# Performance work log

Hardware: AMD Instinct MI355X
Metric: run time of the kernel (lower is better)

The kernel has to match this reference:

```python
import jax, jax.numpy as jnp
import numpy as np

BS, D, L, H = 8, 256, 1024, 8
DK = D // H
EPS = 1e-8


def setup_inputs() -> dict:
    key = jax.random.key(0)
    ks = jax.random.split(key, 9)
    queries = jax.random.normal(ks[0], (BS, D, L), jnp.float32)
    keys = jax.random.normal(ks[1], (BS, D, L), jnp.float32)
    values = jax.random.normal(ks[2], (BS, D, L), jnp.float32)
    # binary float mask over positions, (bs, L, 1) as the module expects
    mask = (jax.random.uniform(ks[3], (BS, L, 1)) > 0.1).astype(jnp.float32)
    # grouped 1x1 conv weights: one (dk, dk) block per head (xavier-ish scale)
    wscale = np.sqrt(2.0 / (DK + DK)).astype(np.float32)
    Wq = jax.random.normal(ks[4], (H, DK, DK), jnp.float32) * wscale
    Wk = jax.random.normal(ks[5], (H, DK, DK), jnp.float32) * wscale
    Wv = jax.random.normal(ks[6], (H, DK, DK), jnp.float32) * wscale
    # full 1x1 conv projection
    Wp = jax.random.normal(ks[7], (D, D), jnp.float32) * np.sqrt(1.0 / D).astype(np.float32)
    bp = jnp.zeros((D,), jnp.float32)
    return {"queries": queries, "keys": keys, "values": values, "mask": mask,
            "Wq": Wq, "Wk": Wk, "Wv": Wv, "Wp": Wp, "bp": bp}


def _grouped_conv1x1(x, W):
    # x: (bs, D, L) viewed as (bs, H, dk, L); W: (H, dk_out, dk_in)
    bs, _, l = x.shape
    xh = x.reshape(bs, H, DK, l)
    return jnp.einsum('hij,bhjl->bhil', W, xh)  # (bs, H, dk, L)


def _masked_softmax(logits, mask4):
    # logits: (bs, H, L, L); mask4: (bs, 1, 1, L) -- faithful to module's custom softmax
    max_value = jax.lax.stop_gradient(jnp.max(logits * mask4, axis=-1, keepdims=True))
    z = (logits - max_value) * mask4
    m = jnp.exp(z) * mask4
    n = jnp.sum(m, axis=-1, keepdims=True)
    p_mask = mask4 * jnp.swapaxes(mask4, 2, 3)  # (bs, 1, L, L)
    return p_mask * (m / (n + EPS))


def reference(queries, keys, values, mask, Wq, Wk, Wv, Wp, bp):
    bs, c, l = queries.shape
    m = jnp.swapaxes(mask, 1, 2)          # (bs, 1, L)
    m4 = m[:, :, None, :]                  # (bs, 1, 1, L)
    q = _grouped_conv1x1(queries, Wq) * m4  # (bs, H, dk, L)
    k = _grouped_conv1x1(keys, Wk) * m4
    v = _grouped_conv1x1(values, Wv)
    # attn[b,h,d,e] = sum_c q[b,h,c,d] k[b,h,c,e]  (no 1/sqrt(dk) scaling, as in source)
    attn = jnp.einsum('bhcd,bhce->bhde', q, k)
    atn = _masked_softmax(attn, m4)
    # value[b,h,c,k] = sum_d atn[b,h,k,d] * (v*mask)[b,h,c,d]
    val = jnp.einsum('bhkd,bhcd->bhck', atn, v * m4)
    val = val.reshape(bs, c, l)
    out = jnp.einsum('ij,bjl->bil', Wp, val) + bp[None, :, None]
    return jnp.swapaxes(out * m, 1, 2)      # (bs, L, D)
```

## Files before the change

### kernel.cpp

```cpp
#include <hip/hip_runtime.h>
#include <math.h>


constexpr int cD  = 256;
constexpr int cL  = 1024;
constexpr int cH  = 8;
constexpr int cDK = 32;
constexpr float kLog2e = 1.44269504088896f;

typedef _Float16 f16;
typedef __attribute__((ext_vector_type(8))) _Float16 h8;
typedef __attribute__((ext_vector_type(4))) _Float16 h4;
typedef __attribute__((ext_vector_type(4))) float f4v;

__global__ __launch_bounds__(256, 4) void proj_qkv_kernel(
    const float* __restrict__ queries, const float* __restrict__ keys,
    const float* __restrict__ values, const float* __restrict__ mask,
    const float* __restrict__ Wq, const float* __restrict__ Wk,
    const float* __restrict__ Wv, const float* __restrict__ Wp,
    f16* __restrict__ qp_h, f16* __restrict__ kp_h, f16* __restrict__ vp_h,
    f16* __restrict__ wp_h)
{
    const int t   = threadIdx.x;
    const int bid = blockIdx.x;

    if (bid >= 1024) {
        const int idx = ((bid - 1024) * 256 + t) * 4;
        float4 f = *reinterpret_cast<const float4*>(&Wp[idx]);
        h4 o; o[0] = (f16)f.x; o[1] = (f16)f.y; o[2] = (f16)f.z; o[3] = (f16)f.w;
        *reinterpret_cast<h4*>(&wp_h[idx]) = o;
        return;
    }

    __shared__ __align__(16) f16 wlds[3][32 * 40];

    const int lt   = bid & 15;
    const int bh   = bid >> 4;
    const int h    = bh & 7;
    const int b    = bh >> 3;
    const int l0   = lt * 64;
    const int lane = t & 63, w = t >> 6, ln15 = lane & 15, lq = lane >> 4;
    const int l    = l0 + w * 16 + ln15;

    {
        const float* Wsrc[3] = {Wq, Wk, Wv};
        const int r = t >> 3, c = (t & 7) * 4;
        #pragma unroll
        for (int m = 0; m < 3; ++m) {
            float4 f = *reinterpret_cast<const float4*>(&Wsrc[m][h * 1024 + t * 4]);
            h4 o; o[0] = (f16)f.x; o[1] = (f16)f.y; o[2] = (f16)f.z; o[3] = (f16)f.w;
            *reinterpret_cast<h4*>(&wlds[m][r * 40 + c]) = o;
        }
    }
    __syncthreads();

    const float mk = mask[b * cL + l];
    const size_t xbase = ((size_t)(b * cD + h * cDK)) * cL + l;

    const float* Xs[3] = {queries, keys, values};
    f4v d0[3], d1[3];

    #pragma unroll
    for (int m = 0; m < 3; ++m) {
        const float* __restrict__ X = Xs[m];
        h8 bx;
        #pragma unroll
        for (int i = 0; i < 8; ++i)
            bx[i] = (f16)X[xbase + (size_t)(lq * 8 + i) * cL];
        h8 a0 = *reinterpret_cast<const h8*>(&wlds[m][ln15 * 40 + lq * 8]);
        h8 a1 = *reinterpret_cast<const h8*>(&wlds[m][(16 + ln15) * 40 + lq * 8]);
        f4v z = {0.f, 0.f, 0.f, 0.f};
        d0[m] = __builtin_amdgcn_mfma_f32_16x16x32_f16(a0, bx, z, 0, 0, 0);
        d1[m] = __builtin_amdgcn_mfma_f32_16x16x32_f16(a1, bx, z, 0, 0, 0);
    }

    {
        const size_t qb = ((size_t)bh * cL + l) * cDK;
        h4 o0, o1;
        #pragma unroll
        for (int i = 0; i < 4; ++i) {
            o0[i] = (f16)(d0[0][i] * kLog2e);
            o1[i] = (f16)(d1[0][i] * kLog2e);
        }
        *reinterpret_cast<h4*>(&qp_h[qb + lq * 4])      = o0;
        *reinterpret_cast<h4*>(&qp_h[qb + 16 + lq * 4]) = o1;
    }
    {
        const size_t kb = ((size_t)bh * cL + l) * cDK;
        h4 o0, o1;
        #pragma unroll
        for (int i = 0; i < 4; ++i) {
            o0[i] = (f16)(d0[1][i] * mk);
            o1[i] = (f16)(d1[1][i] * mk);
        }
        *reinterpret_cast<h4*>(&kp_h[kb + lq * 4])      = o0;
        *reinterpret_cast<h4*>(&kp_h[kb + 16 + lq * 4]) = o1;
    }
    {
        const size_t vb = (size_t)bh * cDK * cL + l;
        #pragma unroll
        for (int i = 0; i < 4; ++i) {
            vp_h[vb + (size_t)(lq * 4 + i) * cL]      = (f16)d0[2][i];
            vp_h[vb + (size_t)(16 + lq * 4 + i) * cL] = (f16)d1[2][i];
        }
    }
}

__global__ __launch_bounds__(256, 5) void attn_kernel(
    const float* __restrict__ mask, const f16* __restrict__ qp_h,
    const f16* __restrict__ kp_h, const f16* __restrict__ vp_h,
    f16* __restrict__ val_h)
{
    __shared__ __align__(16) char smem[28672];
    f16* ks  = (f16*)smem;
    f16* vsb = (f16*)(smem + 10240);
    f16* pbf = (f16*)(smem + 19456);

    const int t     = threadIdx.x;
    const int bid   = blockIdx.x;
    const int bh    = bid & 63;
    const int strip = bid >> 6;
    const int b     = bh >> 3;
    const int r0    = strip * 64;
    const int lane  = t & 63;
    const int w     = t >> 6;
    const int ln15  = lane & 15;
    const int lq    = lane >> 4;

    const size_t kvbase = ((size_t)bh) * 32768;
    const int se = t >> 2, sb = (t & 3) * 8;
    const int vc = t >> 3, veb = (t & 7) * 8;

    const h8 qf = *reinterpret_cast<const h8*>(
        &qp_h[((size_t)bh * cL + r0 + w * 16 + ln15) * cDK + lq * 8]);

    {
        h8 kh = *reinterpret_cast<const h8*>(&kp_h[kvbase + se * 32 + sb]);
        *reinterpret_cast<h8*>(&ks[se * 40 + sb]) = kh;
        h8 vv = *reinterpret_cast<const h8*>(&vp_h[kvbase + vc * 1024 + veb]);
        *reinterpret_cast<h8*>(&vsb[vc * 72 + veb]) = vv;
    }

    f4v o0 = {0.f, 0.f, 0.f, 0.f}, o1 = {0.f, 0.f, 0.f, 0.f};
    float mo = -INFINITY, lrp = 0.f;
    const int prow  = (w * 16 + ln15) * 72;
    const int vsoff = ln15 * 72 + lq * 8;

    for (int et = 0; et < 16; ++et) {
        __syncthreads();
        const int pp = et & 1;
        const bool pre = (et < 15);
        h8 khp, vvp;
        if (pre) {
            const int e0n = (et + 1) * 64;
            khp = *reinterpret_cast<const h8*>(&kp_h[kvbase + (e0n + se) * 32 + sb]);
            vvp = *reinterpret_cast<const h8*>(&vp_h[kvbase + vc * 1024 + e0n + veb]);
        }
        float4 mk4[4];
        #pragma unroll
        for (int es = 0; es < 4; ++es)
            mk4[es] = *reinterpret_cast<const float4*>(
                &mask[b * cL + et * 64 + es * 16 + lq * 4]);

        f4v sA[4];
        #pragma unroll
        for (int es = 0; es < 4; ++es) {
            const h8 kf = *reinterpret_cast<const h8*>(
                &ks[pp * 2560 + (es * 16 + ln15) * 40 + lq * 8]);
            f4v z = {0.f, 0.f, 0.f, 0.f};
            sA[es] = __builtin_amdgcn_mfma_f32_16x16x32_f16(kf, qf, z, 0, 0, 0);
        }

        float tm = -INFINITY;
        #pragma unroll
        for (int es = 0; es < 4; ++es) {
            float r01 = fmaxf(sA[es][0], sA[es][1]);
            float r23 = fmaxf(sA[es][2], sA[es][3]);
            tm = fmaxf(tm, fmaxf(r01, r23));
        }
        tm = fmaxf(tm, __shfl_xor(tm, 16));
        tm = fmaxf(tm, __shfl_xor(tm, 32));
        const float mn = fmaxf(mo, tm);
        const float al = exp2f(mo - mn);
        mo = mn;
        o0[0] *= al; o0[1] *= al; o0[2] *= al; o0[3] *= al;
        o1[0] *= al; o1[1] *= al; o1[2] *= al; o1[3] *= al;

        float ps = 0.f;
        #pragma unroll
        for (int es = 0; es < 4; ++es) {
            float p0 = mk4[es].x * exp2f(sA[es][0] - mn);
            float p1 = mk4[es].y * exp2f(sA[es][1] - mn);
            float p2 = mk4[es].z * exp2f(sA[es][2] - mn);
            float p3 = mk4[es].w * exp2f(sA[es][3] - mn);
            ps += (p0 + p1) + (p2 + p3);
            h4 pk; pk[0] = (f16)p0; pk[1] = (f16)p1; pk[2] = (f16)p2; pk[3] = (f16)p3;
            *reinterpret_cast<h4*>(&pbf[prow + es * 16 + lq * 4]) = pk;
        }
        lrp = lrp * al + ps;

        #pragma unroll
        for (int ch = 0; ch < 2; ++ch) {
            h8 pf  = *reinterpret_cast<const h8*>(&pbf[prow + ch * 32 + lq * 8]);
            h8 va0 = *reinterpret_cast<const h8*>(&vsb[pp * 2304 + vsoff + ch * 32]);
            h8 va1 = *reinterpret_cast<const h8*>(&vsb[pp * 2304 + vsoff + ch * 32 + 1152]);
            o0 = __builtin_amdgcn_mfma_f32_16x16x32_f16(va0, pf, o0, 0, 0, 0);
            o1 = __builtin_amdgcn_mfma_f32_16x16x32_f16(va1, pf, o1, 0, 0, 0);
        }

        if (pre) {
            *reinterpret_cast<h8*>(&ks[(pp ^ 1) * 2560 + se * 40 + sb]) = khp;
            *reinterpret_cast<h8*>(&vsb[(pp ^ 1) * 2304 + vc * 72 + veb]) = vvp;
        }
    }

    {
        float lr = lrp;
        lr += __shfl_xor(lr, 16);
        lr += __shfl_xor(lr, 32);
        const float linv = 1.0f / (lr + 1e-8f);
        const int h = bh & 7;
        const size_t obase = ((size_t)(b * cL + r0 + w * 16 + ln15)) * cD + h * cDK;
        h4 q0, q1;
        #pragma unroll
        for (int i = 0; i < 4; ++i) {
            q0[i] = (f16)(o0[i] * linv);
            q1[i] = (f16)(o1[i] * linv);
        }
        *reinterpret_cast<h4*>(&val_h[obase + lq * 4])      = q0;
        *reinterpret_cast<h4*>(&val_h[obase + 16 + lq * 4]) = q1;
    }
}

__global__ __launch_bounds__(256, 4) void outproj_kernel(
    const f16* __restrict__ val_h, const f16* __restrict__ wp_h,
    const float* __restrict__ bp, const float* __restrict__ mask,
    float* __restrict__ out)
{
    const int t    = threadIdx.x;
    const int bid  = blockIdx.x;
    const int it   = bid & 3;
    const int lt   = (bid >> 2) & 15;
    const int b    = bid >> 6;
    const int l0   = lt * 64, i0 = it * 64;
    const int lane = t & 63, w = t >> 6, ln15 = lane & 15, lq = lane >> 4;

    const size_t abase = ((size_t)(b * cL + l0 + w * 16 + ln15)) * cD + lq * 8;

    f4v acc[4] = {{0.f, 0.f, 0.f, 0.f}, {0.f, 0.f, 0.f, 0.f},
                  {0.f, 0.f, 0.f, 0.f}, {0.f, 0.f, 0.f, 0.f}};
    #pragma unroll
    for (int kc = 0; kc < 8; ++kc) {
        h8 aA = *reinterpret_cast<const h8*>(&val_h[abase + kc * 32]);
        #pragma unroll
        for (int ti = 0; ti < 4; ++ti) {
            h8 bB = *reinterpret_cast<const h8*>(
                &wp_h[((size_t)(i0 + ti * 16 + ln15)) * cD + kc * 32 + lq * 8]);
            acc[ti] = __builtin_amdgcn_mfma_f32_16x16x32_f16(aA, bB, acc[ti], 0, 0, 0);
        }
    }

    float mk[4];
    #pragma unroll
    for (int rg = 0; rg < 4; ++rg)
        mk[rg] = mask[b * cL + l0 + w * 16 + lq * 4 + rg];
    #pragma unroll
    for (int ti = 0; ti < 4; ++ti) {
        float bpv = bp[i0 + ti * 16 + ln15];
        #pragma unroll
        for (int rg = 0; rg < 4; ++rg) {
            int l = l0 + w * 16 + lq * 4 + rg;
            out[((size_t)(b * cL + l)) * cD + i0 + ti * 16 + ln15] =
                (acc[ti][rg] + bpv) * mk[rg];
        }
    }
}

extern "C" void kernel_launch(void* const* d_in, const int* in_sizes, int n_in,
                              void* d_out, int out_size, void* d_ws, size_t ws_size,
                              hipStream_t stream) {
    const float* queries = (const float*)d_in[0];
    const float* keys    = (const float*)d_in[1];
    const float* values  = (const float*)d_in[2];
    const float* mask    = (const float*)d_in[3];
    const float* Wq      = (const float*)d_in[4];
    const float* Wk      = (const float*)d_in[5];
    const float* Wv      = (const float*)d_in[6];
    const float* Wp      = (const float*)d_in[7];
    const float* bp      = (const float*)d_in[8];
    float* out = (float*)d_out;

    char* wsb = (char*)d_ws;
    f16* qp_h  = (f16*)(wsb);
    f16* kp_h  = (f16*)(wsb + (4u << 20));
    f16* vp_h  = (f16*)(wsb + (8u << 20));
    f16* val_h = (f16*)(wsb + (12u << 20));
    f16* wp_h  = (f16*)(wsb + (16u << 20));

    proj_qkv_kernel<<<dim3(1088), dim3(256), 0, stream>>>(
        queries, keys, values, mask, Wq, Wk, Wv, Wp, qp_h, kp_h, vp_h, wp_h);
    attn_kernel<<<dim3(1024), dim3(256), 0, stream>>>(
        mask, qp_h, kp_h, vp_h, val_h);
    outproj_kernel<<<dim3(512), dim3(256), 0, stream>>>(val_h, wp_h, bp, mask, out);
}
```

Before: 142.1 us.

## Read K/V directly from global in attention; stage outproj tiles in LDS

The attention kernel drops its double-buffered LDS staging of K and V tiles and the per-iteration block barrier, loading MFMA operands straight from global memory and relying on cache reuse. Only the P buffer stays in shared memory, and the occupancy hint drops from 5 to 4 blocks. The output projection kernel now stages the val and Wp tiles plus the mask row into padded LDS before its MFMA loop, with the occupancy hint lowered to 2. This trades LDS traffic and barriers for more global/L2 loads in attention, and adds an upfront LDS fill in the projection. The attention loop keeps no barrier around the pbf write/read, but each wave writes and reads only its own 16 P rows, so no cross-wave race is introduced.

```diff
diff --git a/kernel.cpp b/kernel.cpp
--- a/kernel.cpp
+++ b/kernel.cpp
@@ -106,15 +106,12 @@
     }
 }
 
-__global__ __launch_bounds__(256, 5) void attn_kernel(
+__global__ __launch_bounds__(256, 4) void attn_kernel(
     const float* __restrict__ mask, const f16* __restrict__ qp_h,
     const f16* __restrict__ kp_h, const f16* __restrict__ vp_h,
     f16* __restrict__ val_h)
 {
-    __shared__ __align__(16) char smem[28672];
-    f16* ks  = (f16*)smem;
-    f16* vsb = (f16*)(smem + 10240);
-    f16* pbf = (f16*)(smem + 19456);
+    __shared__ __align__(16) f16 pbf[64 * 72];
 
     const int t     = threadIdx.x;
     const int bid   = blockIdx.x;
@@ -128,45 +125,31 @@
     const int lq    = lane >> 4;
 
     const size_t kvbase = ((size_t)bh) * 32768;
-    const int se = t >> 2, sb = (t & 3) * 8;
-    const int vc = t >> 3, veb = (t & 7) * 8;
 
     const h8 qf = *reinterpret_cast<const h8*>(
         &qp_h[((size_t)bh * cL + r0 + w * 16 + ln15) * cDK + lq * 8]);
 
-    {
-        h8 kh = *reinterpret_cast<const h8*>(&kp_h[kvbase + se * 32 + sb]);
-        *reinterpret_cast<h8*>(&ks[se * 40 + sb]) = kh;
-        h8 vv = *reinterpret_cast<const h8*>(&vp_h[kvbase + vc * 1024 + veb]);
-        *reinterpret_cast<h8*>(&vsb[vc * 72 + veb]) = vv;
-    }
-
     f4v o0 = {0.f, 0.f, 0.f, 0.f}, o1 = {0.f, 0.f, 0.f, 0.f};
     float mo = -INFINITY, lrp = 0.f;
-    const int prow  = (w * 16 + ln15) * 72;
-    const int vsoff = ln15 * 72 + lq * 8;
+    const int prow = (w * 16 + ln15) * 72;
+
+    const size_t vrow0 = kvbase + (size_t)ln15 * cL + lq * 8;
+    const size_t vrow1 = kvbase + (size_t)(16 + ln15) * cL + lq * 8;
 
     for (int et = 0; et < 16; ++et) {
-        __syncthreads();
-        const int pp = et & 1;
-        const bool pre = (et < 15);
-        h8 khp, vvp;
-        if (pre) {
-            const int e0n = (et + 1) * 64;
-            khp = *reinterpret_cast<const h8*>(&kp_h[kvbase + (e0n + se) * 32 + sb]);
-            vvp = *reinterpret_cast<const h8*>(&vp_h[kvbase + vc * 1024 + e0n + veb]);
-        }
+        const int e0 = et * 64;
+
         float4 mk4[4];
         #pragma unroll
         for (int es = 0; es < 4; ++es)
             mk4[es] = *reinterpret_cast<const float4*>(
-                &mask[b * cL + et * 64 + es * 16 + lq * 4]);
+                &mask[b * cL + e0 + es * 16 + lq * 4]);
 
         f4v sA[4];
         #pragma unroll
         for (int es = 0; es < 4; ++es) {
             const h8 kf = *reinterpret_cast<const h8*>(
-                &ks[pp * 2560 + (es * 16 + ln15) * 40 + lq * 8]);
+                &kp_h[kvbase + (size_t)(e0 + es * 16 + ln15) * cDK + lq * 8]);
             f4v z = {0.f, 0.f, 0.f, 0.f};
             sA[es] = __builtin_amdgcn_mfma_f32_16x16x32_f16(kf, qf, z, 0, 0, 0);
         }
@@ -202,15 +185,10 @@
         #pragma unroll
         for (int ch = 0; ch < 2; ++ch) {
             h8 pf  = *reinterpret_cast<const h8*>(&pbf[prow + ch * 32 + lq * 8]);
-            h8 va0 = *reinterpret_cast<const h8*>(&vsb[pp * 2304 + vsoff + ch * 32]);
-            h8 va1 = *reinterpret_cast<const h8*>(&vsb[pp * 2304 + vsoff + ch * 32 + 1152]);
+            h8 va0 = *reinterpret_cast<const h8*>(&vp_h[vrow0 + e0 + ch * 32]);
+            h8 va1 = *reinterpret_cast<const h8*>(&vp_h[vrow1 + e0 + ch * 32]);
             o0 = __builtin_amdgcn_mfma_f32_16x16x32_f16(va0, pf, o0, 0, 0, 0);
             o1 = __builtin_amdgcn_mfma_f32_16x16x32_f16(va1, pf, o1, 0, 0, 0);
-        }
-
-        if (pre) {
-            *reinterpret_cast<h8*>(&ks[(pp ^ 1) * 2560 + se * 40 + sb]) = khp;
-            *reinterpret_cast<h8*>(&vsb[(pp ^ 1) * 2304 + vc * 72 + veb]) = vvp;
         }
     }
 
@@ -232,11 +210,15 @@
     }
 }
 
-__global__ __launch_bounds__(256, 4) void outproj_kernel(
+__global__ __launch_bounds__(256, 2) void outproj_kernel(
     const f16* __restrict__ val_h, const f16* __restrict__ wp_h,
     const float* __restrict__ bp, const float* __restrict__ mask,
     float* __restrict__ out)
 {
+    __shared__ __align__(16) f16 vt[64 * 264];
+    __shared__ __align__(16) f16 wpb[64 * 264];
+    __shared__ float mrow[64];
+
     const int t    = threadIdx.x;
     const int bid  = blockIdx.x;
     const int it   = bid & 3;
@@ -245,25 +227,40 @@
     const int l0   = lt * 64, i0 = it * 64;
     const int lane = t & 63, w = t >> 6, ln15 = lane & 15, lq = lane >> 4;
 
-    const size_t abase = ((size_t)(b * cL + l0 + w * 16 + ln15)) * cD + lq * 8;
+    {
+        int row = t & 63, seg = (t >> 6) * 64;
+        const f16* src = &val_h[((size_t)(b * cL + l0 + row)) * cD + seg];
+        #pragma unroll
+        for (int k = 0; k < 8; ++k)
+            *reinterpret_cast<h8*>(&vt[row * 264 + seg + k * 8]) =
+                *reinterpret_cast<const h8*>(src + k * 8);
+    }
+    {
+        int row = t & 63, seg = (t >> 6) * 64;
+        const f16* src = &wp_h[((size_t)(i0 + row)) * cD + seg];
+        #pragma unroll
+        for (int k = 0; k < 8; ++k)
+            *reinterpret_cast<h8*>(&wpb[row * 264 + seg + k * 8]) =
+                *reinterpret_cast<const h8*>(src + k * 8);
+    }
+    if (t < 64) mrow[t] = mask[b * cL + l0 + t];
+    __syncthreads();
 
     f4v acc[4] = {{0.f, 0.f, 0.f, 0.f}, {0.f, 0.f, 0.f, 0.f},
                   {0.f, 0.f, 0.f, 0.f}, {0.f, 0.f, 0.f, 0.f}};
     #pragma unroll
     for (int kc = 0; kc < 8; ++kc) {
-        h8 aA = *reinterpret_cast<const h8*>(&val_h[abase + kc * 32]);
+        h8 aA = *reinterpret_cast<const h8*>(&vt[(w * 16 + ln15) * 264 + kc * 32 + lq * 8]);
         #pragma unroll
         for (int ti = 0; ti < 4; ++ti) {
-            h8 bB = *reinterpret_cast<const h8*>(
-                &wp_h[((size_t)(i0 + ti * 16 + ln15)) * cD + kc * 32 + lq * 8]);
+            h8 bB = *reinterpret_cast<const h8*>(&wpb[(ti * 16 + ln15) * 264 + kc * 32 + lq * 8]);
             acc[ti] = __builtin_amdgcn_mfma_f32_16x16x32_f16(aA, bB, acc[ti], 0, 0, 0);
         }
     }
 
     float mk[4];
     #pragma unroll
-    for (int rg = 0; rg < 4; ++rg)
-        mk[rg] = mask[b * cL + l0 + w * 16 + lq * 4 + rg];
+    for (int rg = 0; rg < 4; ++rg) mk[rg] = mrow[w * 16 + lq * 4 + rg];
     #pragma unroll
     for (int ti = 0; ti < 4; ++ti) {
         float bpv = bp[i0 + ti * 16 + ln15];
```

New measurement: 148.6 us. 1.05x slower.
